# Kernel tuning notes

Measured on AMD Instinct MI355X. Metric: run time of the kernel, lower is better.

The kernel has to match this reference:

```python
import jax, jax.numpy as jnp
import numpy as np

HEADS = 8


def setup_inputs() -> dict:
    key = jax.random.key(0)
    ks = jax.random.split(key, 6)
    b, n, dim = 8, 4096, 512
    s = 0.02
    return {
        "x": jax.random.normal(ks[0], (b, n, dim), jnp.float32),
        "Wq": jax.random.normal(ks[1], (dim, dim), jnp.float32) * s,
        "Wk": jax.random.normal(ks[2], (dim, dim), jnp.float32) * s,
        "Wv": jax.random.normal(ks[3], (dim, dim), jnp.float32) * s,
        "Wo": jax.random.normal(ks[4], (dim, dim), jnp.float32) * s,
        "bo": jnp.zeros((dim,), jnp.float32),
    }


def reference(x, Wq, Wk, Wv, Wo, bo):
    b, n, dim = x.shape
    heads = HEADS
    d = dim // heads
    g = int(np.sqrt(n))  # square grid, n chosen as perfect square (no padding)
    scale = d ** -0.5

    def proj(W):
        # [b, n, dim] -> [b, heads, g, g, d]
        t = jnp.einsum('bne,ef->bnf', x, W)
        return t.reshape(b, g, g, heads, d).transpose(0, 3, 1, 2, 4)

    q, k, v = proj(Wq), proj(Wk), proj(Wv)

    # row-wise attention: attend along last grid axis for each row i
    dots_row = jnp.einsum('bnijd,bnikd->bnijk', q, k) * scale
    out_row = jnp.einsum('bnijk,bnikd->bnijd', jax.nn.softmax(dots_row, axis=-1), v)

    # column-wise attention (as in source: transpose grid axes, same einsum pattern)
    q_c, k_c, v_c = (t.swapaxes(2, 3) for t in (q, k, v))
    dots_col = jnp.einsum('bnjid,bnkid->bnjik', q_c, k_c) * scale
    out_col = jnp.einsum('bnjik,bnkid->bnjid', jax.nn.softmax(dots_col, axis=-1), v_c)

    out = out_row + out_col.swapaxes(2, 3)  # [b, heads, g, g, d]
    out = out.transpose(0, 2, 3, 1, 4).reshape(b, n, dim)
    return jnp.einsum('bne,ef->bnf', out, Wo) + bo
```

## Files before the change

kernel.cpp:

```cpp
#include <hip/hip_runtime.h>
#include <hip/hip_bf16.h>
#include <stdint.h>


typedef __bf16 bf16_t;
typedef __bf16 bf16x2 __attribute__((ext_vector_type(2)));
typedef __bf16 bf16x4v __attribute__((ext_vector_type(4)));
typedef __bf16 bf16x8 __attribute__((ext_vector_type(8)));
typedef float  f32x4  __attribute__((ext_vector_type(4)));

#define GLD16(gp, lp)                                                                  \
  __builtin_amdgcn_global_load_lds((__attribute__((address_space(1))) const void*)(gp),\
                                   (__attribute__((address_space(3))) void*)(lp),      \
                                   16, 0, 0)

__device__ __forceinline__ float  bf2f(bf16_t x) { return (float)x; }
__device__ __forceinline__ bf16_t f2bf(float x)  { return (bf16_t)x; }

__global__ __launch_bounds__(256) void prep(
    const float* __restrict__ x,
    const float* __restrict__ Wq, const float* __restrict__ Wk,
    const float* __restrict__ Wv, const float* __restrict__ Wo,
    bf16_t* __restrict__ xbf, bf16_t* __restrict__ WT)
{
  __shared__ bf16_t tile[32][33];
  const int bid = blockIdx.x, tid = threadIdx.x;
  if (bid < 16384) {
    const int i = bid * 256 + tid;
    float4 v = ((const float4*)x)[i];
    bf16x4v o;
    o[0] = f2bf(v.x); o[1] = f2bf(v.y); o[2] = f2bf(v.z); o[3] = f2bf(v.w);
    ((bf16x4v*)xbf)[i] = o;
  } else {
    const int k = bid - 16384;
    const int mat = k >> 8;
    const float* W = (mat == 0) ? Wq : (mat == 1) ? Wk : (mat == 2) ? Wv : Wo;
    bf16_t* dst = WT + (size_t)mat * 262144;
    const int bx = k & 15, by = (k >> 4) & 15;
    const int tx = tid & 31, ty = tid >> 5;
    const int x0 = bx * 32, y0 = by * 32;
#pragma unroll
    for (int i = 0; i < 32; i += 8)
      tile[ty + i][tx] = f2bf(W[(size_t)(y0 + ty + i) * 512 + x0 + tx]);
    __syncthreads();
#pragma unroll
    for (int i = 0; i < 32; i += 8)
      dst[(size_t)(x0 + ty + i) * 512 + y0 + tx] = tile[tx][ty + i];
  }
}

template <bool STORE_F32>
__global__ __launch_bounds__(512, 2) void gemm256(
    const bf16_t* __restrict__ A,
    const bf16_t* __restrict__ BT,
    void* __restrict__ Cp,
    const float* __restrict__ bias,
    int Nd)
{
  __shared__ __align__(16) bf16_t smem[65536];
  bf16_t* const sA = smem;
  bf16_t* const sB = smem + 32768;

  const int tid  = threadIdx.x;
  const int lane = tid & 63, w = tid >> 6;
  const int quad = lane >> 4, r16 = lane & 15;
  const int wr = w >> 2, wc = w & 3;
  const int wm = wr * 128, wn = wc * 64;

  const int G = gridDim.x;
  const int l = blockIdx.y * G + blockIdx.x;
  const int xcd = l & 7, slot = l >> 3;
  const int mb = xcd * (gridDim.y >> 3) + slot / G;
  const int nb = slot % G;
  const int m0 = mb * 256, n0 = nb * 256;

  const int srow = tid >> 3;
  const int sseg = (tid & 7) ^ (srow & 7);
  const bf16_t* Ag = A  + (size_t)(m0 + srow) * 512 + sseg * 8;
  const bf16_t* Bg = BT + (size_t)(n0 + srow) * 512 + sseg * 8;
  const int sdst = w * 512;

  GLD16(Bg,           sB + sdst);
  GLD16(Bg + 32768,   sB + 4096  + sdst);
  GLD16(Bg + 65536,   sB + 8192  + sdst);
  GLD16(Bg + 98304,   sB + 12288 + sdst);
  GLD16(Ag,           sA + sdst);
  GLD16(Ag + 32768,   sA + 4096  + sdst);
  GLD16(Ag + 65536,   sA + 8192  + sdst);
  GLD16(Ag + 98304,   sA + 12288 + sdst);

  f32x4 acc[8][4] = {};

  const int xsw   = (r16 & 7) << 4;
  const int koff0 = (quad * 16) ^ xsw;
  const int koff1 = (64 + quad * 16) ^ xsw;

  bf16x8 bk[2][4];
  bf16x8 a[2][2];

#define RD_B(dst, base, kof)                                                     \
  _Pragma("unroll") for (int j_ = 0; j_ < 4; ++j_)                               \
    dst[j_] = *(const bf16x8*)((base) + (size_t)(wn + j_ * 16 + r16) * 128 + (kof));
#define RD_A2(dst, base, rowoff, kof)                                            \
  _Pragma("unroll") for (int i_ = 0; i_ < 2; ++i_)                               \
    dst[i_] = *(const bf16x8*)((base) + (size_t)(wm + (rowoff) + i_ * 16 + r16) * 128 + (kof));
#define MFMA8(r0, r1, av, bv)                                                    \
  __builtin_amdgcn_s_setprio(1);                                                 \
  _Pragma("unroll") for (int j_ = 0; j_ < 4; ++j_) {                             \
    acc[r0][j_] = __builtin_amdgcn_mfma_f32_16x16x32_bf16(av[0], bv[j_], acc[r0][j_], 0, 0, 0); \
    acc[r1][j_] = __builtin_amdgcn_mfma_f32_16x16x32_bf16(av[1], bv[j_], acc[r1][j_], 0, 0, 0); \
  }                                                                              \
  __builtin_amdgcn_s_setprio(0);

  asm volatile("s_waitcnt vmcnt(0)" ::: "memory");
  __builtin_amdgcn_s_barrier();

  RD_B(bk[0], (const char*)sB, koff0);
  RD_A2(a[0], (const char*)sA, 0, koff0);

#pragma unroll
  for (int t = 0; t < 8; ++t) {
    const int p = t & 1, pn = p ^ 1;
    const char* sAp  = (const char*)(sA + p  * 16384);
    const char* sBp  = (const char*)(sB + p  * 16384);
    const char* sApn = (const char*)(sA + pn * 16384);
    const char* sBpn = (const char*)(sB + pn * 16384);

    if (t < 7) {
      const int kn = (t + 1) * 64;
      bf16_t* const dA = sA + pn * 16384 + sdst;
      bf16_t* const dB = sB + pn * 16384 + sdst;
      GLD16(Bg + kn,          dB);
      GLD16(Bg + kn + 32768,  dB + 4096);
      GLD16(Bg + kn + 65536,  dB + 8192);
      GLD16(Bg + kn + 98304,  dB + 12288);
      GLD16(Ag + kn,          dA);
      GLD16(Ag + kn + 32768,  dA + 4096);
      GLD16(Ag + kn + 65536,  dA + 8192);
      GLD16(Ag + kn + 98304,  dA + 12288);
    }
    RD_A2(a[1], sAp, 32, koff0);
    MFMA8(0, 1, a[0], bk[0]);

    RD_A2(a[0], sAp, 64, koff0);
    MFMA8(2, 3, a[1], bk[0]);

    RD_A2(a[1], sAp, 96, koff0);
    MFMA8(4, 5, a[0], bk[0]);

    RD_B(bk[1], sBp, koff1);
    RD_A2(a[0], sAp, 0, koff1);
    MFMA8(6, 7, a[1], bk[0]);

    RD_A2(a[1], sAp, 32, koff1);
    MFMA8(0, 1, a[0], bk[1]);

    RD_A2(a[0], sAp, 64, koff1);
    MFMA8(2, 3, a[1], bk[1]);

    RD_A2(a[1], sAp, 96, koff1);
    MFMA8(4, 5, a[0], bk[1]);

    if (t < 7) {
      asm volatile("s_waitcnt vmcnt(0)" ::: "memory");
      __builtin_amdgcn_s_barrier();
      RD_B(bk[0], sBpn, koff0);
      RD_A2(a[0], sApn, 0, koff0);
    }
    MFMA8(6, 7, a[1], bk[1]);
  }

  __syncthreads();

  if (STORE_F32) {
    float* C = (float*)Cp;
#pragma unroll
    for (int i8 = 0; i8 < 8; ++i8) {
#pragma unroll
      for (int j = 0; j < 4; ++j) {
        const int row = m0 + wm + i8 * 16 + quad * 4;
        const int col = n0 + wn + j * 16 + r16;
        const float bv = bias ? bias[col] : 0.0f;
#pragma unroll
        for (int rg = 0; rg < 4; ++rg)
          C[(size_t)(row + rg) * Nd + col] = acc[i8][j][rg] + bv;
      }
    }
  } else {
    bf16_t* Es = smem;
    bf16_t* C  = (bf16_t*)Cp;
#pragma unroll
    for (int pr = 0; pr < 2; ++pr) {
      if (pr) __syncthreads();
      if (wr == pr) {
#pragma unroll
        for (int i8 = 0; i8 < 8; ++i8)
#pragma unroll
          for (int j = 0; j < 4; ++j)
#pragma unroll
            for (int rg = 0; rg < 4; ++rg)
              Es[(size_t)(i8 * 16 + quad * 4 + rg) * 264 + wn + j * 16 + r16] =
                  f2bf(acc[i8][j][rg]);
      }
      __syncthreads();
#pragma unroll
      for (int ps = 0; ps < 8; ++ps) {
        const int row = ps * 16 + (tid >> 5);
        const int cs  = (tid & 31) * 8;
        *(bf16x8*)&C[(size_t)(m0 + pr * 128 + row) * Nd + n0 + cs] =
            *(const bf16x8*)&Es[(size_t)row * 264 + cs];
      }
    }
  }
#undef RD_B
#undef RD_A2
#undef MFMA8
}

__global__ __launch_bounds__(256) void cc_attn(
    const bf16_t* __restrict__ QKV, bf16_t* __restrict__ Aout)
{
  __shared__ __align__(16) bf16_t Qs[64 * 72];
  __shared__ __align__(16) bf16_t Ks[64 * 72];
  __shared__ __align__(16) bf16_t VsT[64 * 70];
  __shared__ __align__(16) bf16_t Ps[64 * 72];

  const int gidx = blockIdx.x;
  const int r = gidx & 63, h = (gidx >> 6) & 7, b = gidx >> 9;
  const int tid = threadIdx.x, lane = tid & 63, w = tid >> 6;
  const int quad = lane >> 4, r16 = lane & 15;
  const size_t row0 = (size_t)b * 4096 + (size_t)r * 64;

  {
    const int row = tid >> 2, seg = tid & 3;
    const bf16_t* gp = QKV + (row0 + row) * 1536 + h * 64 + seg * 16;
    *(bf16x8*)&Qs[row * 72 + seg * 16]     = *(const bf16x8*)&gp[0];
    *(bf16x8*)&Qs[row * 72 + seg * 16 + 8] = *(const bf16x8*)&gp[8];
    *(bf16x8*)&Ks[row * 72 + seg * 16]     = *(const bf16x8*)&gp[512];
    *(bf16x8*)&Ks[row * 72 + seg * 16 + 8] = *(const bf16x8*)&gp[520];
  }
  {
    const int r2 = (tid >> 3) * 2, s8 = tid & 7;
    const bf16_t* gv = QKV + (row0 + r2) * 1536 + h * 64 + 1024 + s8 * 8;
    bf16x8 vA = *(const bf16x8*)&gv[0];
    bf16x8 vB = *(const bf16x8*)&gv[1536];
#pragma unroll
    for (int e = 0; e < 8; ++e) {
      bf16x2 pr; pr[0] = vA[e]; pr[1] = vB[e];
      *(bf16x2*)&VsT[(s8 * 8 + e) * 70 + r2] = pr;
    }
  }
  __syncthreads();

  f32x4 sacc[4] = {};
#pragma unroll
  for (int ks = 0; ks < 2; ++ks) {
    bf16x8 aq = *(const bf16x8*)&Qs[(w * 16 + r16) * 72 + ks * 32 + quad * 8];
#pragma unroll
    for (int nj = 0; nj < 4; ++nj) {
      bf16x8 bkf = *(const bf16x8*)&Ks[(nj * 16 + r16) * 72 + ks * 32 + quad * 8];
      sacc[nj] = __builtin_amdgcn_mfma_f32_16x16x32_bf16(aq, bkf, sacc[nj], 0, 0, 0);
    }
  }

  float ex[4][4];
  float sm[4];
#pragma unroll
  for (int rg = 0; rg < 4; ++rg) {
    float m = -3.0e38f;
#pragma unroll
    for (int nj = 0; nj < 4; ++nj) {
      ex[nj][rg] = sacc[nj][rg] * 0.125f;
      m = fmaxf(m, ex[nj][rg]);
    }
    m = fmaxf(m, __shfl_xor(m, 1));
    m = fmaxf(m, __shfl_xor(m, 2));
    m = fmaxf(m, __shfl_xor(m, 4));
    m = fmaxf(m, __shfl_xor(m, 8));
    float s = 0.f;
#pragma unroll
    for (int nj = 0; nj < 4; ++nj) { ex[nj][rg] = __expf(ex[nj][rg] - m); s += ex[nj][rg]; }
    s += __shfl_xor(s, 1);
    s += __shfl_xor(s, 2);
    s += __shfl_xor(s, 4);
    s += __shfl_xor(s, 8);
    sm[rg] = 2.0f / s;
  }

#pragma unroll
  for (int nj = 0; nj < 4; ++nj)
#pragma unroll
    for (int rg = 0; rg < 4; ++rg)
      Ps[(w * 16 + quad * 4 + rg) * 72 + nj * 16 + r16] = f2bf(ex[nj][rg] * sm[rg]);

  f32x4 oacc[4] = {};
#pragma unroll
  for (int ks = 0; ks < 2; ++ks) {
    bf16x8 ap = *(const bf16x8*)&Ps[(w * 16 + r16) * 72 + ks * 32 + quad * 8];
#pragma unroll
    for (int nj = 0; nj < 4; ++nj) {
      bf16x8 bv = *(const bf16x8*)&VsT[(nj * 16 + r16) * 70 + ks * 32 + quad * 8];
      oacc[nj] = __builtin_amdgcn_mfma_f32_16x16x32_bf16(ap, bv, oacc[nj], 0, 0, 0);
    }
  }

  {
    bf16_t* Es = Qs;
#pragma unroll
    for (int nj = 0; nj < 4; ++nj)
#pragma unroll
      for (int rg = 0; rg < 4; ++rg)
        Es[(w * 16 + quad * 4 + rg) * 72 + nj * 16 + r16] = f2bf(oacc[nj][rg]);
    __syncthreads();
    const size_t obase = row0 * 512 + (size_t)h * 64;
#pragma unroll
    for (int rd = 0; rd < 2; ++rd) {
      const int row = rd * 32 + (tid >> 3);
      const int col = (tid & 7) * 8;
      *(bf16x8*)&Aout[obase + (size_t)row * 512 + col] = *(const bf16x8*)&Es[row * 72 + col];
    }
  }
}

extern "C" void kernel_launch(void* const* d_in, const int* in_sizes, int n_in,
                              void* d_out, int out_size, void* d_ws, size_t ws_size,
                              hipStream_t stream)
{
  const float* x  = (const float*)d_in[0];
  const float* Wq = (const float*)d_in[1];
  const float* Wk = (const float*)d_in[2];
  const float* Wv = (const float*)d_in[3];
  const float* Wo = (const float*)d_in[4];
  const float* bo = (const float*)d_in[5];

  bf16_t* ws = (bf16_t*)d_ws;
  bf16_t* WT  = ws;
  bf16_t* xbf = ws + 1048576;
  bf16_t* QKV = xbf + 16777216;
  bf16_t* Ab  = xbf;

  prep<<<dim3(17408), 256, 0, stream>>>(x, Wq, Wk, Wv, Wo, xbf, WT);

  gemm256<false><<<dim3(6, 128), 512, 0, stream>>>(xbf, WT, QKV, nullptr, 1536);

  cc_attn<<<dim3(4096), 256, 0, stream>>>(QKV, Ab);

  gemm256<true><<<dim3(2, 128), 512, 0, stream>>>(Ab, WT + 786432, d_out, bo, 512);
}
```

Before: 233.4 us.

## Fuse criss-cross attention with output projection in one per-row-block kernel

Each block now processes one 64-token grid row across all 8 heads, one wave per head. Q and K fragments are loaded straight from global memory into registers instead of going through LDS. The per-head attention outputs are staged in LDS as a 64x512 tile and multiplied by Wo in the same block, with bias added and fp32 written directly. This removes the bf16 attention-output round trip through global memory and the separate Wo GEMM launch. In exchange the grid drops to 512 blocks, register use rises, and every block re-reads Wo from global/L2 without LDS tiling.

```diff
diff --git a/kernel.cpp b/kernel.cpp
--- a/kernel.cpp
+++ b/kernel.cpp
@@ -217,109 +217,140 @@
 #undef MFMA8
 }
 
-__global__ __launch_bounds__(256) void cc_attn(
-    const bf16_t* __restrict__ QKV, bf16_t* __restrict__ Aout)
+__global__ __launch_bounds__(512) void cc_attn_o(
+    const bf16_t* __restrict__ QKV, const bf16_t* __restrict__ WoT,
+    const float* __restrict__ bo, float* __restrict__ Out)
 {
-  __shared__ __align__(16) bf16_t Qs[64 * 72];
-  __shared__ __align__(16) bf16_t Ks[64 * 72];
-  __shared__ __align__(16) bf16_t VsT[64 * 70];
-  __shared__ __align__(16) bf16_t Ps[64 * 72];
-
+  __shared__ __align__(16) bf16_t smem[46080];
   const int gidx = blockIdx.x;
-  const int r = gidx & 63, h = (gidx >> 6) & 7, b = gidx >> 9;
+  const int r = gidx & 63, b = gidx >> 6;
   const int tid = threadIdx.x, lane = tid & 63, w = tid >> 6;
   const int quad = lane >> 4, r16 = lane & 15;
   const size_t row0 = (size_t)b * 4096 + (size_t)r * 64;
 
-  {
-    const int row = tid >> 2, seg = tid & 3;
-    const bf16_t* gp = QKV + (row0 + row) * 1536 + h * 64 + seg * 16;
-    *(bf16x8*)&Qs[row * 72 + seg * 16]     = *(const bf16x8*)&gp[0];
-    *(bf16x8*)&Qs[row * 72 + seg * 16 + 8] = *(const bf16x8*)&gp[8];
-    *(bf16x8*)&Ks[row * 72 + seg * 16]     = *(const bf16x8*)&gp[512];
-    *(bf16x8*)&Ks[row * 72 + seg * 16 + 8] = *(const bf16x8*)&gp[520];
-  }
-  {
-    const int r2 = (tid >> 3) * 2, s8 = tid & 7;
-    const bf16_t* gv = QKV + (row0 + r2) * 1536 + h * 64 + 1024 + s8 * 8;
-    bf16x8 vA = *(const bf16x8*)&gv[0];
-    bf16x8 vB = *(const bf16x8*)&gv[1536];
+  bf16_t* const VsT = smem + w * 4608;
+  bf16_t* const Ps  = smem + 36864 + w * 1152;
+
+  const bf16_t* qb = QKV + row0 * 1536 + w * 64;
+
+  bf16x8 aq[4][2], kb[4][2];
+#pragma unroll
+  for (int fi = 0; fi < 4; ++fi)
+#pragma unroll
+    for (int ks = 0; ks < 2; ++ks) {
+      aq[fi][ks] = *(const bf16x8*)&qb[(size_t)(fi * 16 + r16) * 1536 + ks * 32 + quad * 8];
+      kb[fi][ks] = *(const bf16x8*)&qb[(size_t)(fi * 16 + r16) * 1536 + 512 + ks * 32 + quad * 8];
+    }
+  const int r2 = (lane & 31) * 2, hf = lane >> 5;
+  const bf16_t* vb = qb + 1024 + hf * 32;
+  bf16x8 v0[4], v1[4];
+#pragma unroll
+  for (int e8 = 0; e8 < 4; ++e8) {
+    v0[e8] = *(const bf16x8*)&vb[(size_t)r2 * 1536 + e8 * 8];
+    v1[e8] = *(const bf16x8*)&vb[(size_t)(r2 + 1) * 1536 + e8 * 8];
+  }
+
+  f32x4 sacc[4][4] = {};
+#pragma unroll
+  for (int ks = 0; ks < 2; ++ks)
+#pragma unroll
+    for (int fi = 0; fi < 4; ++fi)
+#pragma unroll
+      for (int nj = 0; nj < 4; ++nj)
+        sacc[fi][nj] = __builtin_amdgcn_mfma_f32_16x16x32_bf16(
+            aq[fi][ks], kb[nj][ks], sacc[fi][nj], 0, 0, 0);
+
+#pragma unroll
+  for (int e8 = 0; e8 < 4; ++e8)
 #pragma unroll
     for (int e = 0; e < 8; ++e) {
-      bf16x2 pr; pr[0] = vA[e]; pr[1] = vB[e];
-      *(bf16x2*)&VsT[(s8 * 8 + e) * 70 + r2] = pr;
-    }
-  }
+      bf16x2 pr; pr[0] = v0[e8][e]; pr[1] = v1[e8][e];
+      *(bf16x2*)&VsT[(hf * 32 + e8 * 8 + e) * 72 + r2] = pr;
+    }
+
+  f32x4 oacc[4][4] = {};
+#pragma unroll
+  for (int fi = 0; fi < 4; ++fi) {
+    float ex[4][4], sm[4];
+#pragma unroll
+    for (int rg = 0; rg < 4; ++rg) {
+      float m = -3.0e38f;
+#pragma unroll
+      for (int nj = 0; nj < 4; ++nj) {
+        ex[nj][rg] = sacc[fi][nj][rg] * 0.125f;
+        m = fmaxf(m, ex[nj][rg]);
+      }
+      m = fmaxf(m, __shfl_xor(m, 1));
+      m = fmaxf(m, __shfl_xor(m, 2));
+      m = fmaxf(m, __shfl_xor(m, 4));
+      m = fmaxf(m, __shfl_xor(m, 8));
+      float s = 0.f;
+#pragma unroll
+      for (int nj = 0; nj < 4; ++nj) { ex[nj][rg] = __expf(ex[nj][rg] - m); s += ex[nj][rg]; }
+      s += __shfl_xor(s, 1);
+      s += __shfl_xor(s, 2);
+      s += __shfl_xor(s, 4);
+      s += __shfl_xor(s, 8);
+      sm[rg] = 2.0f / s;
+    }
+#pragma unroll
+    for (int nj = 0; nj < 4; ++nj)
+#pragma unroll
+      for (int rg = 0; rg < 4; ++rg)
+        Ps[(quad * 4 + rg) * 72 + nj * 16 + r16] = f2bf(ex[nj][rg] * sm[rg]);
+
+    bf16x8 ap0 = *(const bf16x8*)&Ps[r16 * 72 + quad * 8];
+    bf16x8 ap1 = *(const bf16x8*)&Ps[r16 * 72 + 32 + quad * 8];
+#pragma unroll
+    for (int nj = 0; nj < 4; ++nj) {
+      bf16x8 bv0 = *(const bf16x8*)&VsT[(nj * 16 + r16) * 72 + quad * 8];
+      bf16x8 bv1 = *(const bf16x8*)&VsT[(nj * 16 + r16) * 72 + 32 + quad * 8];
+      oacc[fi][nj] = __builtin_amdgcn_mfma_f32_16x16x32_bf16(ap0, bv0, oacc[fi][nj], 0, 0, 0);
+      oacc[fi][nj] = __builtin_amdgcn_mfma_f32_16x16x32_bf16(ap1, bv1, oacc[fi][nj], 0, 0, 0);
+    }
+  }
+
   __syncthreads();
-
-  f32x4 sacc[4] = {};
-#pragma unroll
-  for (int ks = 0; ks < 2; ++ks) {
-    bf16x8 aq = *(const bf16x8*)&Qs[(w * 16 + r16) * 72 + ks * 32 + quad * 8];
+  bf16_t* const Oc = smem;
+#pragma unroll
+  for (int fi = 0; fi < 4; ++fi)
+#pragma unroll
+    for (int nj = 0; nj < 4; ++nj)
+#pragma unroll
+      for (int rg = 0; rg < 4; ++rg)
+        Oc[(size_t)(fi * 16 + quad * 4 + rg) * 520 + w * 64 + nj * 16 + r16] =
+            f2bf(oacc[fi][nj][rg]);
+  __syncthreads();
+
+  f32x4 c2[4][4] = {};
+  const bf16_t* Bg = WoT + (size_t)(w * 64) * 512;
+#pragma unroll
+  for (int ks = 0; ks < 16; ++ks) {
+    bf16x8 af[4];
+#pragma unroll
+    for (int fi = 0; fi < 4; ++fi)
+      af[fi] = *(const bf16x8*)&Oc[(size_t)(fi * 16 + r16) * 520 + ks * 32 + quad * 8];
 #pragma unroll
     for (int nj = 0; nj < 4; ++nj) {
-      bf16x8 bkf = *(const bf16x8*)&Ks[(nj * 16 + r16) * 72 + ks * 32 + quad * 8];
-      sacc[nj] = __builtin_amdgcn_mfma_f32_16x16x32_bf16(aq, bkf, sacc[nj], 0, 0, 0);
-    }
-  }
-
-  float ex[4][4];
-  float sm[4];
-#pragma unroll
-  for (int rg = 0; rg < 4; ++rg) {
-    float m = -3.0e38f;
+      bf16x8 bf_ = *(const bf16x8*)&Bg[(size_t)(nj * 16 + r16) * 512 + ks * 32 + quad * 8];
+#pragma unroll
+      for (int fi = 0; fi < 4; ++fi)
+        c2[fi][nj] = __builtin_amdgcn_mfma_f32_16x16x32_bf16(af[fi], bf_, c2[fi][nj], 0, 0, 0);
+    }
+  }
+
+#pragma unroll
+  for (int fi = 0; fi < 4; ++fi)
 #pragma unroll
     for (int nj = 0; nj < 4; ++nj) {
-      ex[nj][rg] = sacc[nj][rg] * 0.125f;
-      m = fmaxf(m, ex[nj][rg]);
-    }
-    m = fmaxf(m, __shfl_xor(m, 1));
-    m = fmaxf(m, __shfl_xor(m, 2));
-    m = fmaxf(m, __shfl_xor(m, 4));
-    m = fmaxf(m, __shfl_xor(m, 8));
-    float s = 0.f;
-#pragma unroll
-    for (int nj = 0; nj < 4; ++nj) { ex[nj][rg] = __expf(ex[nj][rg] - m); s += ex[nj][rg]; }
-    s += __shfl_xor(s, 1);
-    s += __shfl_xor(s, 2);
-    s += __shfl_xor(s, 4);
-    s += __shfl_xor(s, 8);
-    sm[rg] = 2.0f / s;
-  }
-
-#pragma unroll
-  for (int nj = 0; nj < 4; ++nj)
-#pragma unroll
-    for (int rg = 0; rg < 4; ++rg)
-      Ps[(w * 16 + quad * 4 + rg) * 72 + nj * 16 + r16] = f2bf(ex[nj][rg] * sm[rg]);
-
-  f32x4 oacc[4] = {};
-#pragma unroll
-  for (int ks = 0; ks < 2; ++ks) {
-    bf16x8 ap = *(const bf16x8*)&Ps[(w * 16 + r16) * 72 + ks * 32 + quad * 8];
-#pragma unroll
-    for (int nj = 0; nj < 4; ++nj) {
-      bf16x8 bv = *(const bf16x8*)&VsT[(nj * 16 + r16) * 70 + ks * 32 + quad * 8];
-      oacc[nj] = __builtin_amdgcn_mfma_f32_16x16x32_bf16(ap, bv, oacc[nj], 0, 0, 0);
-    }
-  }
-
-  {
-    bf16_t* Es = Qs;
-#pragma unroll
-    for (int nj = 0; nj < 4; ++nj)
-#pragma unroll
-      for (int rg = 0; rg < 4; ++rg)
-        Es[(w * 16 + quad * 4 + rg) * 72 + nj * 16 + r16] = f2bf(oacc[nj][rg]);
-    __syncthreads();
-    const size_t obase = row0 * 512 + (size_t)h * 64;
-#pragma unroll
-    for (int rd = 0; rd < 2; ++rd) {
-      const int row = rd * 32 + (tid >> 3);
-      const int col = (tid & 7) * 8;
-      *(bf16x8*)&Aout[obase + (size_t)row * 512 + col] = *(const bf16x8*)&Es[row * 72 + col];
-    }
-  }
+      const int col = w * 64 + nj * 16 + r16;
+      const float bv = bo[col];
+#pragma unroll
+      for (int rg = 0; rg < 4; ++rg) {
+        const size_t row = row0 + fi * 16 + quad * 4 + rg;
+        Out[row * 512 + col] = c2[fi][nj][rg] + bv;
+      }
+    }
 }
 
 extern "C" void kernel_launch(void* const* d_in, const int* in_sizes, int n_in,
@@ -337,13 +368,10 @@
   bf16_t* WT  = ws;
   bf16_t* xbf = ws + 1048576;
   bf16_t* QKV = xbf + 16777216;
-  bf16_t* Ab  = xbf;
 
   prep<<<dim3(17408), 256, 0, stream>>>(x, Wq, Wk, Wv, Wo, xbf, WT);
 
   gemm256<false><<<dim3(6, 128), 512, 0, stream>>>(xbf, WT, QKV, nullptr, 1536);
 
-  cc_attn<<<dim3(4096), 256, 0, stream>>>(QKV, Ab);
-
-  gemm256<true><<<dim3(2, 128), 512, 0, stream>>>(Ab, WT + 786432, d_out, bo, 512);
+  cc_attn_o<<<dim3(512), 512, 0, stream>>>(QKV, WT + 786432, bo, (float*)d_out);
 }
```

Result: slower. 255.3 us (+9.4%).

## Fuse fp32-to-bf16 input conversion into QKV GEMM A-tile loading

Applied to the files above, without the earlier changes.

The separate prep pass that converted x to bf16 is removed; the QKV GEMM now loads fp32 A tiles into registers, converts them, and stores bf16 into LDS, double-buffered across k steps. Weight transposition moves to a small dedicated kernel. This removes one full read/write pass over the activations and a kernel launch. In exchange, each GEMM block re-reads A as fp32, doubling A traffic across the N-blocks, and replaces async global-to-LDS loads with register staging plus full barriers.

```diff
diff --git a/kernel.cpp b/kernel.cpp
--- a/kernel.cpp
+++ b/kernel.cpp
@@ -17,41 +17,28 @@
 __device__ __forceinline__ float  bf2f(bf16_t x) { return (float)x; }
 __device__ __forceinline__ bf16_t f2bf(float x)  { return (bf16_t)x; }
 
-__global__ __launch_bounds__(256) void prep(
-    const float* __restrict__ x,
-    const float* __restrict__ Wq, const float* __restrict__ Wk,
-    const float* __restrict__ Wv, const float* __restrict__ Wo,
-    bf16_t* __restrict__ xbf, bf16_t* __restrict__ WT)
+__global__ void wt_kernel(const float* __restrict__ Wq, const float* __restrict__ Wk,
+                          const float* __restrict__ Wv, const float* __restrict__ Wo,
+                          bf16_t* __restrict__ WT)
 {
   __shared__ bf16_t tile[32][33];
-  const int bid = blockIdx.x, tid = threadIdx.x;
-  if (bid < 16384) {
-    const int i = bid * 256 + tid;
-    float4 v = ((const float4*)x)[i];
-    bf16x4v o;
-    o[0] = f2bf(v.x); o[1] = f2bf(v.y); o[2] = f2bf(v.z); o[3] = f2bf(v.w);
-    ((bf16x4v*)xbf)[i] = o;
-  } else {
-    const int k = bid - 16384;
-    const int mat = k >> 8;
-    const float* W = (mat == 0) ? Wq : (mat == 1) ? Wk : (mat == 2) ? Wv : Wo;
-    bf16_t* dst = WT + (size_t)mat * 262144;
-    const int bx = k & 15, by = (k >> 4) & 15;
-    const int tx = tid & 31, ty = tid >> 5;
-    const int x0 = bx * 32, y0 = by * 32;
-#pragma unroll
-    for (int i = 0; i < 32; i += 8)
-      tile[ty + i][tx] = f2bf(W[(size_t)(y0 + ty + i) * 512 + x0 + tx]);
-    __syncthreads();
-#pragma unroll
-    for (int i = 0; i < 32; i += 8)
-      dst[(size_t)(x0 + ty + i) * 512 + y0 + tx] = tile[tx][ty + i];
-  }
+  const int mat = blockIdx.z;
+  const float* W = (mat == 0) ? Wq : (mat == 1) ? Wk : (mat == 2) ? Wv : Wo;
+  bf16_t* dst = WT + (size_t)mat * 262144;
+  const int tx = threadIdx.x, ty = threadIdx.y;
+  const int x0 = blockIdx.x * 32, y0 = blockIdx.y * 32;
+#pragma unroll
+  for (int i = 0; i < 32; i += 8)
+    tile[ty + i][tx] = f2bf(W[(size_t)(y0 + ty + i) * 512 + x0 + tx]);
+  __syncthreads();
+#pragma unroll
+  for (int i = 0; i < 32; i += 8)
+    dst[(size_t)(x0 + ty + i) * 512 + y0 + tx] = tile[tx][ty + i];
 }
 
-template <bool STORE_F32>
+template <bool A_F32, bool STORE_F32>
 __global__ __launch_bounds__(512, 2) void gemm256(
-    const bf16_t* __restrict__ A,
+    const void* __restrict__ Aptr,
     const bf16_t* __restrict__ BT,
     void* __restrict__ Cp,
     const float* __restrict__ bias,
@@ -76,18 +63,12 @@
 
   const int srow = tid >> 3;
   const int sseg = (tid & 7) ^ (srow & 7);
-  const bf16_t* Ag = A  + (size_t)(m0 + srow) * 512 + sseg * 8;
-  const bf16_t* Bg = BT + (size_t)(n0 + srow) * 512 + sseg * 8;
+  const float*  Af  = (const float*)Aptr;
+  const bf16_t* Abf = (const bf16_t*)Aptr;
+  const float*  Agf = Af  + (size_t)(m0 + srow) * 512 + sseg * 8;
+  const bf16_t* Agb = Abf + (size_t)(m0 + srow) * 512 + sseg * 8;
+  const bf16_t* Bg  = BT  + (size_t)(n0 + srow) * 512 + sseg * 8;
   const int sdst = w * 512;
-
-  GLD16(Bg,           sB + sdst);
-  GLD16(Bg + 32768,   sB + 4096  + sdst);
-  GLD16(Bg + 65536,   sB + 8192  + sdst);
-  GLD16(Bg + 98304,   sB + 12288 + sdst);
-  GLD16(Ag,           sA + sdst);
-  GLD16(Ag + 32768,   sA + 4096  + sdst);
-  GLD16(Ag + 65536,   sA + 8192  + sdst);
-  GLD16(Ag + 98304,   sA + 12288 + sdst);
 
   f32x4 acc[8][4] = {};
 
@@ -111,9 +92,41 @@
     acc[r1][j_] = __builtin_amdgcn_mfma_f32_16x16x32_bf16(av[1], bv[j_], acc[r1][j_], 0, 0, 0); \
   }                                                                              \
   __builtin_amdgcn_s_setprio(0);
-
-  asm volatile("s_waitcnt vmcnt(0)" ::: "memory");
-  __builtin_amdgcn_s_barrier();
+#define LDA_F32(avv, c_, kn_)                                                    \
+  avv[2*(c_)]   = *(const float4*)&Agf[(size_t)(c_) * 32768 + (kn_)];            \
+  avv[2*(c_)+1] = *(const float4*)&Agf[(size_t)(c_) * 32768 + (kn_) + 4];
+#define STA_F32(avv, dApn)                                                       \
+  _Pragma("unroll") for (int c_ = 0; c_ < 4; ++c_) {                             \
+    bf16x8 o_;                                                                   \
+    o_[0] = f2bf(avv[2*c_].x);   o_[1] = f2bf(avv[2*c_].y);                      \
+    o_[2] = f2bf(avv[2*c_].z);   o_[3] = f2bf(avv[2*c_].w);                      \
+    o_[4] = f2bf(avv[2*c_+1].x); o_[5] = f2bf(avv[2*c_+1].y);                    \
+    o_[6] = f2bf(avv[2*c_+1].z); o_[7] = f2bf(avv[2*c_+1].w);                    \
+    *(bf16x8*)&(dApn)[c_ * 4096 + tid * 8] = o_;                                 \
+  }
+
+  if constexpr (A_F32) {
+    float4 av0[8];
+#pragma unroll
+    for (int c = 0; c < 4; ++c) { LDA_F32(av0, c, 0) }
+    GLD16(Bg,           sB + sdst);
+    GLD16(Bg + 32768,   sB + 4096  + sdst);
+    GLD16(Bg + 65536,   sB + 8192  + sdst);
+    GLD16(Bg + 98304,   sB + 12288 + sdst);
+    STA_F32(av0, sA)
+    __syncthreads();
+  } else {
+    GLD16(Bg,            sB + sdst);
+    GLD16(Bg + 32768,    sB + 4096  + sdst);
+    GLD16(Bg + 65536,    sB + 8192  + sdst);
+    GLD16(Bg + 98304,    sB + 12288 + sdst);
+    GLD16(Agb,           sA + sdst);
+    GLD16(Agb + 32768,   sA + 4096  + sdst);
+    GLD16(Agb + 65536,   sA + 8192  + sdst);
+    GLD16(Agb + 98304,   sA + 12288 + sdst);
+    asm volatile("s_waitcnt vmcnt(0)" ::: "memory");
+    __builtin_amdgcn_s_barrier();
+  }
 
   RD_B(bk[0], (const char*)sB, koff0);
   RD_A2(a[0], (const char*)sA, 0, koff0);
@@ -125,19 +138,30 @@
     const char* sBp  = (const char*)(sB + p  * 16384);
     const char* sApn = (const char*)(sA + pn * 16384);
     const char* sBpn = (const char*)(sB + pn * 16384);
+    bf16_t* const dA = sA + pn * 16384;
+    bf16_t* const dB = sB + pn * 16384 + sdst;
+    const int kn = (t + 1) * 64;
+    float4 av[8];
 
     if (t < 7) {
-      const int kn = (t + 1) * 64;
-      bf16_t* const dA = sA + pn * 16384 + sdst;
-      bf16_t* const dB = sB + pn * 16384 + sdst;
-      GLD16(Bg + kn,          dB);
-      GLD16(Bg + kn + 32768,  dB + 4096);
-      GLD16(Bg + kn + 65536,  dB + 8192);
-      GLD16(Bg + kn + 98304,  dB + 12288);
-      GLD16(Ag + kn,          dA);
-      GLD16(Ag + kn + 32768,  dA + 4096);
-      GLD16(Ag + kn + 65536,  dA + 8192);
-      GLD16(Ag + kn + 98304,  dA + 12288);
+      if constexpr (A_F32) {
+#pragma unroll
+        for (int c = 0; c < 4; ++c) { LDA_F32(av, c, kn) }
+        GLD16(Bg + kn,          dB);
+        GLD16(Bg + kn + 32768,  dB + 4096);
+        GLD16(Bg + kn + 65536,  dB + 8192);
+        GLD16(Bg + kn + 98304,  dB + 12288);
+      } else {
+        bf16_t* const dAb = sA + pn * 16384 + sdst;
+        GLD16(Bg + kn,           dB);
+        GLD16(Bg + kn + 32768,   dB + 4096);
+        GLD16(Bg + kn + 65536,   dB + 8192);
+        GLD16(Bg + kn + 98304,   dB + 12288);
+        GLD16(Agb + kn,          dAb);
+        GLD16(Agb + kn + 32768,  dAb + 4096);
+        GLD16(Agb + kn + 65536,  dAb + 8192);
+        GLD16(Agb + kn + 98304,  dAb + 12288);
+      }
     }
     RD_A2(a[1], sAp, 32, koff0);
     MFMA8(0, 1, a[0], bk[0]);
@@ -155,6 +179,9 @@
     RD_A2(a[1], sAp, 32, koff1);
     MFMA8(0, 1, a[0], bk[1]);
 
+    if (t < 7) {
+      if constexpr (A_F32) { STA_F32(av, dA) }
+    }
     RD_A2(a[0], sAp, 64, koff1);
     MFMA8(2, 3, a[1], bk[1]);
 
@@ -162,8 +189,12 @@
     MFMA8(4, 5, a[0], bk[1]);
 
     if (t < 7) {
-      asm volatile("s_waitcnt vmcnt(0)" ::: "memory");
-      __builtin_amdgcn_s_barrier();
+      if constexpr (A_F32) {
+        __syncthreads();
+      } else {
+        asm volatile("s_waitcnt vmcnt(0)" ::: "memory");
+        __builtin_amdgcn_s_barrier();
+      }
       RD_B(bk[0], sBpn, koff0);
       RD_A2(a[0], sApn, 0, koff0);
     }
@@ -215,6 +246,8 @@
 #undef RD_B
 #undef RD_A2
 #undef MFMA8
+#undef LDA_F32
+#undef STA_F32
 }
 
 __global__ __launch_bounds__(256) void cc_attn(
@@ -335,15 +368,14 @@
 
   bf16_t* ws = (bf16_t*)d_ws;
   bf16_t* WT  = ws;
-  bf16_t* xbf = ws + 1048576;
-  bf16_t* QKV = xbf + 16777216;
-  bf16_t* Ab  = xbf;
-
-  prep<<<dim3(17408), 256, 0, stream>>>(x, Wq, Wk, Wv, Wo, xbf, WT);
-
-  gemm256<false><<<dim3(6, 128), 512, 0, stream>>>(xbf, WT, QKV, nullptr, 1536);
+  bf16_t* Ab  = ws + 1048576;
+  bf16_t* QKV = Ab + 16777216;
+
+  wt_kernel<<<dim3(16, 16, 4), dim3(32, 8), 0, stream>>>(Wq, Wk, Wv, Wo, WT);
+
+  gemm256<true, false><<<dim3(6, 128), 512, 0, stream>>>(x, WT, QKV, nullptr, 1536);
 
   cc_attn<<<dim3(4096), 256, 0, stream>>>(QKV, Ab);
 
-  gemm256<true><<<dim3(2, 128), 512, 0, stream>>>(Ab, WT + 786432, d_out, bo, 512);
+  gemm256<false, true><<<dim3(2, 128), 512, 0, stream>>>(Ab, WT + 786432, d_out, bo, 512);
 }
```

Result: slower. 248.1 us (+6.3%).
